# Kernel optimization log

Measured on AMD Instinct MI355X. Metric: run time of the kernel, lower is better.

## Reference

```python
import jax, jax.numpy as jnp
import numpy as np

N, C, H, W = 4, 128, 64, 64


def setup_inputs() -> dict:
    key = jax.random.key(0)
    ks = jax.random.split(key, 4)
    s = 1.0 / np.sqrt(C).astype(np.float32)  # conv2d default-init scale
    return {
        "x": jax.random.normal(ks[0], (N, C, H, W), dtype=jnp.float32),
        "Wq": jax.random.normal(ks[1], (C, C), dtype=jnp.float32) * s,
        "bq": jnp.zeros((C,), dtype=jnp.float32),
        "Wk": jax.random.normal(ks[2], (C, C), dtype=jnp.float32) * s,
        "bk": jnp.zeros((C,), dtype=jnp.float32),
        "Wv": jax.random.normal(ks[3], (C, C), dtype=jnp.float32) * s,
        "bv": jnp.zeros((C,), dtype=jnp.float32),
    }


def reference(x, Wq, bq, Wk, bk, Wv, bv):
    n, c, h, w = x.shape
    xf = x.reshape(n, c, h * w)  # [N, C, L], L = H*W
    # 1x1 convs == per-pixel channel mixing
    q = jnp.einsum('oc,ncl->nol', Wq, xf) + bq[:, None]
    k = jnp.einsum('oc,ncl->nol', Wk, xf) + bk[:, None]
    v = jnp.einsum('oc,ncl->nol', Wv, xf) + bv[:, None]
    # scores[l, m] = sum_c k[c,l] * q[c,m]  (matmul(k^T, q))
    scale = jnp.asarray(1.0 / np.sqrt(c), x.dtype)
    scores = jnp.einsum('ncl,ncm->nlm', k, q) * scale  # [N, L, L]
    temp = jax.nn.softmax(scores, axis=-1)
    attn = jnp.einsum('ncl,nlm->ncm', v, temp)  # [N, C, L]
    return x + attn.reshape(n, c, h, w)
```

## Files before the change

### kernel.cpp

```cpp
#include <hip/hip_runtime.h>
#include <hip/hip_bf16.h>
#include <stdint.h>

#define NB 4
#define CH 128
#define LL 4096

typedef __attribute__((ext_vector_type(8))) short short8;
typedef __attribute__((ext_vector_type(4))) short short4b;
typedef __attribute__((ext_vector_type(4))) float floatx4;
typedef __attribute__((ext_vector_type(16))) float floatx16;


static __device__ __forceinline__ short f2bf(float f) {
    uint32_t u = __float_as_uint(f);
    u += 0x7fffu + ((u >> 16) & 1u);
    return (short)(u >> 16);
}
static __device__ __forceinline__ float bf2f(short s) {
    return __uint_as_float(((uint32_t)(uint16_t)s) << 16);
}

__global__ __launch_bounds__(256) void wprep_kernel(
    const float* __restrict__ Wq, const float* __restrict__ Wk,
    const float* __restrict__ Wv, short* __restrict__ Wf)
{
    const int g = blockIdx.x * 256 + threadIdx.x;
    const int mat = g >> 14;
    const int rem = g & 16383;
    const int o   = rem >> 7;
    const int c   = rem & 127;
    const float* W = (mat == 0) ? Wq : (mat == 1) ? Wk : Wv;
    float v = W[o * CH + c];
    if (mat == 1) v *= 0.08838834764831845f;
    Wf[(size_t)mat * 16384 + (o >> 4) * 2048 + (c >> 5) * 512
       + ((c >> 3) & 3) * 128 + (o & 15) * 8 + (c & 7)] = f2bf(v);
}

__global__ __launch_bounds__(256) void proj_kernel(
    const float* __restrict__ x, const short* __restrict__ Wf,
    const float* __restrict__ bq, const float* __restrict__ bk,
    const float* __restrict__ bv,
    short* __restrict__ Qf, short* __restrict__ Kf, short* __restrict__ Vp)
{
    const int i    = blockIdx.x;
    const int n    = (i >> 1) & 3;
    const int lt   = ((i >> 3) << 1) | (i & 1);
    const int l0   = lt << 5;
    const int tid  = threadIdx.x;
    const int wave = tid >> 6;
    const int lane = tid & 63;
    const int quad = lane >> 4;
    const int mc   = lane & 15;

    __shared__ short Xb[32][136];

    {
        const int sl = tid & 31;
        const int cg = tid >> 5;
        const float* xp = x + ((size_t)n * CH + cg * 16) * LL + l0 + sl;
        short8 buf;
        #pragma unroll
        for (int i2 = 0; i2 < 16; ++i2) {
            buf[i2 & 7] = f2bf(xp[(size_t)i2 * LL]);
            if ((i2 & 7) == 7)
                *(short8*)(void*)&Xb[sl][cg * 16 + (i2 & 8)] = buf;
        }
    }
    __syncthreads();

    const int lt2 = wave >> 1;
    const int oh  = wave & 1;
    const int gt  = lt * 2 + lt2;

    short8 xf[4];
    #pragma unroll
    for (int s = 0; s < 4; ++s)
        xf[s] = *(const short8*)(const void*)&Xb[lt2 * 16 + mc][32 * s + quad * 8];

    const size_t obase = ((size_t)n * 256 + gt) * 2048;
    const float scale = 0.08838834764831845f;

    #pragma unroll
    for (int mat = 0; mat < 3; ++mat) {
        const short* Wm = Wf + (size_t)mat * 16384;
        const float* bb = (mat == 0) ? bq : (mat == 1) ? bk : bv;
        const float bscale = (mat == 1) ? scale : 1.0f;
        #pragma unroll
        for (int ot = oh * 4; ot < oh * 4 + 4; ++ot) {
            floatx4 acc = {0.f, 0.f, 0.f, 0.f};
            #pragma unroll
            for (int s = 0; s < 4; ++s)
                acc = __builtin_amdgcn_mfma_f32_16x16x32_bf16(
                    *(const short8*)(const void*)(Wm + ot * 2048 + s * 512 + lane * 8),
                    xf[s], acc, 0, 0, 0);
            const int c0 = ot * 16 + 4 * quad;
            if (mat < 2) {
                short4b pv;
                #pragma unroll
                for (int r = 0; r < 4; ++r)
                    pv[r] = f2bf(acc[r] + bb[c0 + r] * bscale);
                short* dst = ((mat == 0) ? Qf : Kf) + obase
                           + (c0 >> 5) * 512 + ((c0 >> 3) & 3) * 128
                           + mc * 8 + (c0 & 7);
                *(short4b*)(void*)dst = pv;
            } else {
                #pragma unroll
                for (int r = 0; r < 4; ++r)
                    Vp[obase + (c0 + r) * 16 + mc] = f2bf(acc[r] + bb[c0 + r]);
            }
        }
    }
}

__global__ __launch_bounds__(512, 4) void rowsum_kernel(
    const short* __restrict__ Qf, const short* __restrict__ Kf,
    float* __restrict__ Dv)
{
    const int i    = blockIdx.x;
    const int n    = (i >> 1) & 3;
    const int tp   = ((i >> 3) << 1) | (i & 1);
    const int tid  = threadIdx.x;
    const int wave = tid >> 6;
    const int lane = tid & 63;
    const int quad = lane >> 4;
    const int mc   = lane & 15;

    __shared__ float Db[8][32];

    const short* Kb = Kf + ((size_t)n * 256 + tp * 2) * 2048 + lane * 8;
    short8 kf[2][4];
    #pragma unroll
    for (int t = 0; t < 2; ++t)
        #pragma unroll
        for (int s = 0; s < 4; ++s)
            kf[t][s] = *(const short8*)(const void*)(Kb + t * 2048 + s * 512);

    const short* Qn = Qf + (size_t)n * 524288 + (size_t)wave * 32 * 2048 + lane * 8;
    float rs[2][4] = {{0.f, 0.f, 0.f, 0.f}, {0.f, 0.f, 0.f, 0.f}};

    short8 qA[4], qB[4];
    #pragma unroll
    for (int s = 0; s < 4; ++s)
        qA[s] = *(const short8*)(const void*)(Qn + s * 512);

    auto qstep = [&](const short8 (&q)[4]) {
        floatx4 a0 = {0.f, 0.f, 0.f, 0.f};
        floatx4 a1 = {0.f, 0.f, 0.f, 0.f};
        #pragma unroll
        for (int s = 0; s < 4; ++s) {
            a0 = __builtin_amdgcn_mfma_f32_16x16x32_bf16(kf[0][s], q[s], a0, 0, 0, 0);
            a1 = __builtin_amdgcn_mfma_f32_16x16x32_bf16(kf[1][s], q[s], a1, 0, 0, 0);
        }
        #pragma unroll
        for (int r = 0; r < 4; ++r) {
            rs[0][r] += __expf(a0[r]);
            rs[1][r] += __expf(a1[r]);
        }
    };

    for (int it = 0; it < 32; it += 2) {
        #pragma unroll
        for (int s = 0; s < 4; ++s)
            qB[s] = *(const short8*)(const void*)(
                Qn + (size_t)((it + 1) & 31) * 2048 + s * 512);
        qstep(qA);
        #pragma unroll
        for (int s = 0; s < 4; ++s)
            qA[s] = *(const short8*)(const void*)(
                Qn + (size_t)((it + 2) & 31) * 2048 + s * 512);
        qstep(qB);
    }

    #pragma unroll
    for (int t = 0; t < 2; ++t)
        #pragma unroll
        for (int r = 0; r < 4; ++r) {
            float v = rs[t][r];
            v += __shfl_xor(v, 1);
            v += __shfl_xor(v, 2);
            v += __shfl_xor(v, 4);
            v += __shfl_xor(v, 8);
            if (mc == 0) Db[wave][t * 16 + quad * 4 + r] = v;
        }
    __syncthreads();
    if (tid < 32) {
        float s = 0.f;
        #pragma unroll
        for (int m = 0; m < 8; ++m) s += Db[m][tid];
        Dv[(size_t)n * 4096 + tp * 32 + tid] = 1.0f / s;
    }
}

__global__ __launch_bounds__(512, 4) void attn_out_kernel(
    const short* __restrict__ Qf, const short* __restrict__ Kf,
    const short* __restrict__ Vp, const float* __restrict__ Dv,
    float* __restrict__ Po)
{
    const int i    = blockIdx.x;
    const int n    = (i >> 1) & 3;
    const int j    = ((i >> 3) << 1) | (i & 1);
    const int lh   = j >> 6;
    const int mb   = j & 63;
    const int m0   = mb << 6;
    const int tid  = threadIdx.x;
    const int wave = tid >> 6;
    const int lane = tid & 63;
    const int quad = lane >> 4;
    const int mc   = lane & 15;
    const int l32  = lane & 31;
    const int h    = lane >> 5;
    const int ct   = wave & 3;
    const int mh   = wave >> 2;

    __shared__ short P[2][64][264];

    const short* Qn  = Qf + (size_t)n * 524288;
    const short* Kn  = Kf + (size_t)n * 524288;
    const short* Vpn = Vp + (size_t)n * 524288;
    const float* Dn  = Dv + (size_t)n * 4096;
    const int tile0  = lh * 128;

    floatx16 acc;
    #pragma unroll
    for (int r = 0; r < 16; ++r) acc[r] = 0.f;

    for (int t = 0; t < 8; ++t) {
        const int p = t & 1;

        {
            const int tb = tile0 + t * 16 + 2 * wave;
            short8 kfr[2][4];
            #pragma unroll
            for (int jj = 0; jj < 2; ++jj)
                #pragma unroll
                for (int s = 0; s < 4; ++s)
                    kfr[jj][s] = *(const short8*)(const void*)(
                        Kn + (size_t)(tb + jj) * 2048 + s * 512 + lane * 8);
            floatx4 dr[2];
            #pragma unroll
            for (int jj = 0; jj < 2; ++jj)
                dr[jj] = *(const floatx4*)(const void*)(
                    Dn + (tb + jj) * 16 + quad * 4);

            #pragma unroll
            for (int mst = 0; mst < 4; ++mst) {
                short8 qt[4];
                #pragma unroll
                for (int s = 0; s < 4; ++s)
                    qt[s] = *(const short8*)(const void*)(
                        Qn + (size_t)((m0 >> 4) + mst) * 2048 + s * 512 + lane * 8);
                floatx4 sa0 = {0.f, 0.f, 0.f, 0.f};
                floatx4 sa1 = {0.f, 0.f, 0.f, 0.f};
                #pragma unroll
                for (int s = 0; s < 4; ++s) {
                    sa0 = __builtin_amdgcn_mfma_f32_16x16x32_bf16(kfr[0][s], qt[s], sa0, 0, 0, 0);
                    sa1 = __builtin_amdgcn_mfma_f32_16x16x32_bf16(kfr[1][s], qt[s], sa1, 0, 0, 0);
                }
                short4b pv0, pv1;
                #pragma unroll
                for (int r = 0; r < 4; ++r) {
                    pv0[r] = f2bf(__expf(sa0[r]) * dr[0][r]);
                    pv1[r] = f2bf(__expf(sa1[r]) * dr[1][r]);
                }
                *(short4b*)(void*)&P[p][16 * mst + mc][32 * wave + quad * 4] = pv0;
                *(short4b*)(void*)&P[p][16 * mst + mc][32 * wave + 16 + quad * 4] = pv1;
            }
        }
        __syncthreads();

        #pragma unroll
        for (int kc = 0; kc < 16; ++kc) {
            const short8 vf = *(const short8*)(const void*)(
                Vpn + (size_t)(tile0 + t * 16 + kc) * 2048
                    + (32 * ct + l32) * 16 + 8 * h);
            const short8 pf = *(const short8*)(const void*)&P[p][32 * mh + l32][16 * kc + 8 * h];
            acc = __builtin_amdgcn_mfma_f32_32x32x16_bf16(vf, pf, acc, 0, 0, 0);
        }
    }

    float* Pon = Po + (size_t)(lh * 4 + n) * 524288;
    #pragma unroll
    for (int r = 0; r < 16; ++r) {
        const int c = 32 * ct + (r & 3) + 8 * (r >> 2) + 4 * h;
        const int m = m0 + 32 * mh + l32;
        Pon[(size_t)c * LL + m] = acc[r];
    }
}

__global__ __launch_bounds__(256) void combine_kernel(
    const float* __restrict__ x, const float* __restrict__ Po,
    float* __restrict__ out)
{
    const size_t k = (size_t)blockIdx.x * 256 + threadIdx.x;
    const floatx4 a = *(const floatx4*)(const void*)(x + 4 * k);
    const floatx4 b = *(const floatx4*)(const void*)(Po + 4 * k);
    const floatx4 c = *(const floatx4*)(const void*)(Po + 2097152 + 4 * k);
    floatx4 o;
    #pragma unroll
    for (int r = 0; r < 4; ++r) o[r] = a[r] + b[r] + c[r];
    *(floatx4*)(void*)(out + 4 * k) = o;
}

extern "C" void kernel_launch(void* const* d_in, const int* in_sizes, int n_in,
                              void* d_out, int out_size, void* d_ws, size_t ws_size,
                              hipStream_t stream) {
    (void)in_sizes; (void)n_in; (void)out_size; (void)ws_size;
    const float* x  = (const float*)d_in[0];
    const float* Wq = (const float*)d_in[1];
    const float* bq = (const float*)d_in[2];
    const float* Wk = (const float*)d_in[3];
    const float* bk = (const float*)d_in[4];
    const float* Wv = (const float*)d_in[5];
    const float* bv = (const float*)d_in[6];
    float* out = (float*)d_out;

    char* ws = (char*)d_ws;
    short* Qf = (short*)(ws);
    short* Kf = (short*)(ws + 4194304);
    short* Vp = (short*)(ws + 8388608);
    float* Dv = (float*)(ws + 12582912);
    short* Wf = (short*)(ws + 16777216);
    float* Po = (float*)(ws + 16908288);

    wprep_kernel<<<192, 256, 0, stream>>>(Wq, Wk, Wv, Wf);
    proj_kernel<<<512, 256, 0, stream>>>(x, Wf, bq, bk, bv, Qf, Kf, Vp);
    rowsum_kernel<<<512, 512, 0, stream>>>(Qf, Kf, Dv);
    attn_out_kernel<<<512, 512, 0, stream>>>(Qf, Kf, Vp, Dv, Po);
    combine_kernel<<<2048, 256, 0, stream>>>(x, Po, out);
}
```

Baseline: 157.8 us.

## Hoist Q fragments into registers and remap score work across waves

Each wave now owns two 16-column m-subtiles and loads their Q fragments once before the tile loop, keeping them in registers instead of reloading Q every iteration. The wave-to-work mapping for the score MFMAs changes so that each wave handles 4 key tiles by 2 m-subtiles rather than 2 key tiles by 4 m-subtiles. The shared P row padding also shrinks from 264 to 260. This is meant to cut redundant global/L2 Q loads, at the cost of more live registers under 512-thread launch bounds and a different LDS bank pattern.

New measurement: 174.2 us. 10.4% more time.

```diff
diff --git a/kernel.cpp b/kernel.cpp
--- a/kernel.cpp
+++ b/kernel.cpp
@@ -210,10 +210,12 @@
     const int mc   = lane & 15;
     const int l32  = lane & 31;
     const int h    = lane >> 5;
+    const int mq   = wave & 1;
+    const int lq   = wave >> 1;
     const int ct   = wave & 3;
     const int mh   = wave >> 2;
 
-    __shared__ short P[2][64][264];
+    __shared__ short P[2][64][260];
 
     const short* Qn  = Qf + (size_t)n * 524288;
     const short* Kn  = Kf + (size_t)n * 524288;
@@ -221,50 +223,47 @@
     const float* Dn  = Dv + (size_t)n * 4096;
     const int tile0  = lh * 128;
 
+    const size_t vcol = (size_t)(32 * ct + l32) * 16 + 8 * h;
+
+    short8 qf[2][4];
+    #pragma unroll
+    for (int ms = 0; ms < 2; ++ms)
+        #pragma unroll
+        for (int s = 0; s < 4; ++s)
+            qf[ms][s] = *(const short8*)(const void*)(
+                Qn + (size_t)(mb * 4 + mq * 2 + ms) * 2048 + s * 512 + lane * 8);
+
     floatx16 acc;
     #pragma unroll
     for (int r = 0; r < 16; ++r) acc[r] = 0.f;
 
     for (int t = 0; t < 8; ++t) {
-        const int p = t & 1;
-
-        {
-            const int tb = tile0 + t * 16 + 2 * wave;
-            short8 kfr[2][4];
+        const int p   = t & 1;
+        const int tb0 = tile0 + t * 16;
+
+        #pragma unroll
+        for (int tl = 0; tl < 4; ++tl) {
+            const int tb = tb0 + lq * 4 + tl;
+            short8 kfr[4];
             #pragma unroll
-            for (int jj = 0; jj < 2; ++jj)
+            for (int s = 0; s < 4; ++s)
+                kfr[s] = *(const short8*)(const void*)(
+                    Kn + (size_t)tb * 2048 + s * 512 + lane * 8);
+            const floatx4 drt = *(const floatx4*)(const void*)(
+                Dn + tb * 16 + quad * 4);
+
+            #pragma unroll
+            for (int ms = 0; ms < 2; ++ms) {
+                floatx4 sa = {0.f, 0.f, 0.f, 0.f};
                 #pragma unroll
                 for (int s = 0; s < 4; ++s)
-                    kfr[jj][s] = *(const short8*)(const void*)(
-                        Kn + (size_t)(tb + jj) * 2048 + s * 512 + lane * 8);
-            floatx4 dr[2];
-            #pragma unroll
-            for (int jj = 0; jj < 2; ++jj)
-                dr[jj] = *(const floatx4*)(const void*)(
-                    Dn + (tb + jj) * 16 + quad * 4);
-
-            #pragma unroll
-            for (int mst = 0; mst < 4; ++mst) {
-                short8 qt[4];
+                    sa = __builtin_amdgcn_mfma_f32_16x16x32_bf16(kfr[s], qf[ms][s], sa, 0, 0, 0);
+                short4b pv;
                 #pragma unroll
-                for (int s = 0; s < 4; ++s)
-                    qt[s] = *(const short8*)(const void*)(
-                        Qn + (size_t)((m0 >> 4) + mst) * 2048 + s * 512 + lane * 8);
-                floatx4 sa0 = {0.f, 0.f, 0.f, 0.f};
-                floatx4 sa1 = {0.f, 0.f, 0.f, 0.f};
-                #pragma unroll
-                for (int s = 0; s < 4; ++s) {
-                    sa0 = __builtin_amdgcn_mfma_f32_16x16x32_bf16(kfr[0][s], qt[s], sa0, 0, 0, 0);
-                    sa1 = __builtin_amdgcn_mfma_f32_16x16x32_bf16(kfr[1][s], qt[s], sa1, 0, 0, 0);
-                }
-                short4b pv0, pv1;
-                #pragma unroll
-                for (int r = 0; r < 4; ++r) {
-                    pv0[r] = f2bf(__expf(sa0[r]) * dr[0][r]);
-                    pv1[r] = f2bf(__expf(sa1[r]) * dr[1][r]);
-                }
-                *(short4b*)(void*)&P[p][16 * mst + mc][32 * wave + quad * 4] = pv0;
-                *(short4b*)(void*)&P[p][16 * mst + mc][32 * wave + 16 + quad * 4] = pv1;
+                for (int r = 0; r < 4; ++r)
+                    pv[r] = f2bf(__expf(sa[r]) * drt[r]);
+                *(short4b*)(void*)&P[p][16 * (mq * 2 + ms) + mc]
+                                    [(lq * 4 + tl) * 16 + quad * 4] = pv;
             }
         }
         __syncthreads();
@@ -272,8 +271,7 @@
         #pragma unroll
         for (int kc = 0; kc < 16; ++kc) {
             const short8 vf = *(const short8*)(const void*)(
-                Vpn + (size_t)(tile0 + t * 16 + kc) * 2048
-                    + (32 * ct + l32) * 16 + 8 * h);
+                Vpn + (size_t)(tb0 + kc) * 2048 + vcol);
             const short8 pf = *(const short8*)(const void*)&P[p][32 * mh + l32][16 * kc + 8 * h];
             acc = __builtin_amdgcn_mfma_f32_32x32x16_bf16(vf, pf, acc, 0, 0, 0);
         }
```

## Widen rowsum blocks to 1024 threads and retune attention LDS padding

Applied to the files above, without the earlier changes.

The rowsum kernel now runs 256 blocks of 1024 threads, each covering 64 key rows split into two 32-row halves, with all 16 waves sweeping the same Q tiles so that Q reads can be shared through cache. The explicit double-buffered Q prefetch is replaced by a simple loop that loads each tile and uses it immediately, leaving latency hiding to the compiler and to occupancy. The final reduction is adjusted to match the new layout. The attention kernel's LDS row padding changes from 264 to 260 shorts to alter the bank-conflict pattern, which may also break the 16-byte alignment of vector LDS accesses.

Result: slower. 179.2 us (+13.5%).

```diff
diff --git a/kernel.cpp b/kernel.cpp
--- a/kernel.cpp
+++ b/kernel.cpp
@@ -113,22 +113,24 @@
     }
 }
 
-__global__ __launch_bounds__(512, 4) void rowsum_kernel(
+__global__ __launch_bounds__(1024) void rowsum_kernel(
     const short* __restrict__ Qf, const short* __restrict__ Kf,
     float* __restrict__ Dv)
 {
     const int i    = blockIdx.x;
     const int n    = (i >> 1) & 3;
-    const int tp   = ((i >> 3) << 1) | (i & 1);
+    const int tq   = ((i >> 3) << 1) | (i & 1);
     const int tid  = threadIdx.x;
     const int wave = tid >> 6;
     const int lane = tid & 63;
     const int quad = lane >> 4;
     const int mc   = lane & 15;
-
-    __shared__ float Db[8][32];
-
-    const short* Kb = Kf + ((size_t)n * 256 + tp * 2) * 2048 + lane * 8;
+    const int mw   = wave & 7;
+    const int th   = wave >> 3;
+
+    __shared__ float Db[16][32];
+
+    const short* Kb = Kf + ((size_t)n * 256 + tq * 4 + th * 2) * 2048 + lane * 8;
     short8 kf[2][4];
     #pragma unroll
     for (int t = 0; t < 2; ++t)
@@ -136,15 +138,15 @@
         for (int s = 0; s < 4; ++s)
             kf[t][s] = *(const short8*)(const void*)(Kb + t * 2048 + s * 512);
 
-    const short* Qn = Qf + (size_t)n * 524288 + (size_t)wave * 32 * 2048 + lane * 8;
+    const short* Qn = Qf + (size_t)n * 524288 + (size_t)mw * 32 * 2048 + lane * 8;
     float rs[2][4] = {{0.f, 0.f, 0.f, 0.f}, {0.f, 0.f, 0.f, 0.f}};
 
-    short8 qA[4], qB[4];
-    #pragma unroll
-    for (int s = 0; s < 4; ++s)
-        qA[s] = *(const short8*)(const void*)(Qn + s * 512);
-
-    auto qstep = [&](const short8 (&q)[4]) {
+    for (int it = 0; it < 32; ++it) {
+        short8 q[4];
+        #pragma unroll
+        for (int s = 0; s < 4; ++s)
+            q[s] = *(const short8*)(const void*)(
+                Qn + (size_t)it * 2048 + s * 512);
         floatx4 a0 = {0.f, 0.f, 0.f, 0.f};
         floatx4 a1 = {0.f, 0.f, 0.f, 0.f};
         #pragma unroll
@@ -157,19 +159,6 @@
             rs[0][r] += __expf(a0[r]);
             rs[1][r] += __expf(a1[r]);
         }
-    };
-
-    for (int it = 0; it < 32; it += 2) {
-        #pragma unroll
-        for (int s = 0; s < 4; ++s)
-            qB[s] = *(const short8*)(const void*)(
-                Qn + (size_t)((it + 1) & 31) * 2048 + s * 512);
-        qstep(qA);
-        #pragma unroll
-        for (int s = 0; s < 4; ++s)
-            qA[s] = *(const short8*)(const void*)(
-                Qn + (size_t)((it + 2) & 31) * 2048 + s * 512);
-        qstep(qB);
     }
 
     #pragma unroll
@@ -184,11 +173,12 @@
             if (mc == 0) Db[wave][t * 16 + quad * 4 + r] = v;
         }
     __syncthreads();
-    if (tid < 32) {
+    if (tid < 64) {
+        const int lh = tid >> 5, lr = tid & 31;
         float s = 0.f;
         #pragma unroll
-        for (int m = 0; m < 8; ++m) s += Db[m][tid];
-        Dv[(size_t)n * 4096 + tp * 32 + tid] = 1.0f / s;
+        for (int m = 0; m < 8; ++m) s += Db[lh * 8 + m][lr];
+        Dv[(size_t)n * 4096 + tq * 64 + tid] = 1.0f / s;
     }
 }
 
@@ -213,7 +203,7 @@
     const int ct   = wave & 3;
     const int mh   = wave >> 2;
 
-    __shared__ short P[2][64][264];
+    __shared__ short P[2][64][260];
 
     const short* Qn  = Qf + (size_t)n * 524288;
     const short* Kn  = Kf + (size_t)n * 524288;
@@ -325,7 +315,7 @@
 
     wprep_kernel<<<192, 256, 0, stream>>>(Wq, Wk, Wv, Wf);
     proj_kernel<<<512, 256, 0, stream>>>(x, Wf, bq, bk, bv, Qf, Kf, Vp);
-    rowsum_kernel<<<512, 512, 0, stream>>>(Qf, Kf, Dv);
+    rowsum_kernel<<<256, 1024, 0, stream>>>(Qf, Kf, Dv);
     attn_out_kernel<<<512, 512, 0, stream>>>(Qf, Kf, Vp, Dv, Po);
     combine_kernel<<<2048, 256, 0, stream>>>(x, Po, out);
 }
```
